# Kernel optimization log

Measured on AMD Instinct MI355X. Metric: run time of the kernel, lower is better.

The kernel has to match this reference:

```python
import jax, jax.numpy as jnp
import numpy as np

EPS = 1e-08


def _center(K):
    # H K H with H = I - 11^T/n, expressed as O(n^2) double mean-subtraction
    rm = K.mean(axis=-1, keepdims=True)
    cm = K.mean(axis=-2, keepdims=True)
    tm = K.mean(axis=(-1, -2), keepdims=True)
    return K - rm - cm + tm


def setup_inputs() -> dict:
    key = jax.random.key(0)
    k1, k2 = jax.random.split(key)
    L, B, n, d = 5, 8, 1024, 64
    teacher = jax.random.normal(k1, (L, B, n, d), dtype=jnp.float32)
    student = jax.random.normal(k2, (L, B, n, d), dtype=jnp.float32)
    return {"teacher": teacher, "student": student}


def reference(teacher, student):
    # teacher, student: [L, B, n, d]  (internal=True, dim>=3 branch)
    cX = _center(jnp.einsum('lbnd,lbmd->lbnm', teacher, teacher))  # [L,B,n,n]
    cY = _center(jnp.einsum('lbnd,lbmd->lbnm', student, student))  # [L,B,n,n]
    hsic_xy = jnp.sum(cX * cY, axis=(-1, -2))  # [L,B]
    var_x = jnp.sqrt(jnp.sum(cX * cX, axis=(-1, -2)))  # [L,B]
    var_y = jnp.sqrt(jnp.sum(cY * cY, axis=(-1, -2)))  # [L,B]
    ratio = jnp.abs(hsic_xy / (var_x * var_y))  # [L,B]
    loss_per_layer = -jnp.log(ratio.mean(axis=-1) + EPS)  # [L]
    return loss_per_layer.mean()  # sum over layers / length
```

## Files before the change

### kernel.cpp

```cpp
#include <hip/hip_runtime.h>
#include <math.h>

#define LL 5
#define BB 8
#define NN 1024
#define DD 64
#define LB (LL * BB)
#define SPLIT 8
#define ROWS (NN / SPLIT)
#define ZC (2 * DD)

#define G_SZ (LB * SPLIT * ZC * ZC)
#define S_SZ (LB * SPLIT * ZC)
#define ACC_OFF (G_SZ + S_SZ)

typedef short short8 __attribute__((ext_vector_type(8)));
typedef float floatx4 __attribute__((ext_vector_type(4)));

__device__ __forceinline__ unsigned short f2bf(float f) {
    union { float f; unsigned u; } v; v.f = f;
    const unsigned u = v.u;
    return (unsigned short)((u + 0x7FFFu + ((u >> 16) & 1u)) >> 16);
}

__device__ __forceinline__ short8 read_frag(const short* Zt, int t, int lane, int k0) {
    const int c = t + (lane & 15);
    const int o = (k0 >> 3) + (lane >> 4);
    return *(const short8*)(Zt + c * 128 + ((o ^ (c & 15)) << 3));
}

__global__ __launch_bounds__(256) void gram_kernel(const float* __restrict__ X,
                                                   const float* __restrict__ Y,
                                                   float* __restrict__ Gp,
                                                   float* __restrict__ Sp) {
    __shared__ short Zt[128 * 128];
    __shared__ float csum_sh[2][ZC];

    const int lb = blockIdx.y, nc = blockIdx.x, tid = threadIdx.x;
    const int c = tid & 127;
    const int half = tid >> 7;
    const int rbase = nc * ROWS;

    const float* src = (c < DD) ? (X + (size_t)lb * NN * DD + c)
                                : (Y + (size_t)lb * NN * DD + (c - DD));

#pragma unroll 4
    for (int j = 0; j < 32; ++j) {
        const int kp = half * 32 + j;
        const float v0 = src[(size_t)(rbase + 2 * kp) * DD];
        const float v1 = src[(size_t)(rbase + 2 * kp + 1) * DD];
        const unsigned val = (unsigned)f2bf(v0) | ((unsigned)f2bf(v1) << 16);
        const int o = kp >> 2, dw = kp & 3;
        *(unsigned*)((char*)Zt + (c << 8) + ((o ^ (c & 15)) << 4) + (dw << 2)) = val;
    }
    __syncthreads();

    {
        float s = 0.0f;
#pragma unroll
        for (int oo = 0; oo < 8; ++oo) {
            const int o = half * 8 + oo;
            const short8 v = *(const short8*)(Zt + c * 128 + ((o ^ (c & 15)) << 3));
#pragma unroll
            for (int e = 0; e < 8; ++e) {
                union { unsigned u; float f; } t2;
                t2.u = ((unsigned)(unsigned short)v[e]) << 16;
                s += t2.f;
            }
        }
        csum_sh[half][c] = s;
    }
    __syncthreads();
    if (tid < ZC) Sp[(lb * SPLIT + nc) * ZC + tid] = csum_sh[0][tid] + csum_sh[1][tid];

    const int lane = tid & 63, w = tid >> 6;
    const int wr = (w >> 1) * 64, wc = (w & 1) * 64;

    floatx4 acc[4][4];
#pragma unroll
    for (int i = 0; i < 4; ++i)
#pragma unroll
        for (int j = 0; j < 4; ++j)
            acc[i][j] = (floatx4){0.f, 0.f, 0.f, 0.f};

#pragma unroll
    for (int k0 = 0; k0 < ROWS; k0 += 32) {
        short8 af[4], bf_[4];
#pragma unroll
        for (int i = 0; i < 4; ++i) af[i] = read_frag(Zt, wr + i * 16, lane, k0);
#pragma unroll
        for (int j = 0; j < 4; ++j) bf_[j] = read_frag(Zt, wc + j * 16, lane, k0);
#pragma unroll
        for (int i = 0; i < 4; ++i)
#pragma unroll
            for (int j = 0; j < 4; ++j)
                acc[i][j] = __builtin_amdgcn_mfma_f32_16x16x32_bf16(af[i], bf_[j], acc[i][j], 0, 0, 0);
    }

    float* Gb = Gp + (size_t)(lb * SPLIT + nc) * (ZC * ZC);
    const int g = lane >> 4, cl = lane & 15;
#pragma unroll
    for (int i = 0; i < 4; ++i)
#pragma unroll
        for (int j = 0; j < 4; ++j)
#pragma unroll
            for (int r = 0; r < 4; ++r)
                Gb[(wr + i * 16 + g * 4 + r) * ZC + (wc + j * 16 + cl)] = acc[i][j][r];
}

__global__ __launch_bounds__(256) void reduce_kernel(const float* __restrict__ Gp,
                                                     const float* __restrict__ Sp,
                                                     float* __restrict__ Acc) {
    const int lb = blockIdx.x >> 2;
    const int q = blockIdx.x & 3;
    const int tid = threadIdx.x;
    __shared__ float s_sh[ZC];
    __shared__ float red[3][4];

    if (tid < ZC) {
        float s = 0.0f;
#pragma unroll
        for (int sp = 0; sp < SPLIT; ++sp) s += Sp[(lb * SPLIT + sp) * ZC + tid];
        s_sh[tid] = s;
    }
    __syncthreads();

    const float4* Gp4 = (const float4*)Gp;
    const size_t lb_base = (size_t)lb * SPLIT * (ZC * ZC / 4);
    float vxx = 0.0f, vyy = 0.0f, hxy = 0.0f;
    const float inv_n = 1.0f / (float)NN;
#pragma unroll
    for (int k = 0; k < 4; ++k) {
        const int e4 = q * 1024 + k * 256 + tid;
        float4 gsum = make_float4(0.f, 0.f, 0.f, 0.f);
#pragma unroll
        for (int sp = 0; sp < SPLIT; ++sp) {
            const float4 p = Gp4[lb_base + (size_t)sp * (ZC * ZC / 4) + e4];
            gsum.x += p.x; gsum.y += p.y; gsum.z += p.z; gsum.w += p.w;
        }
        const int i = e4 >> 5;
        const int j0 = (e4 & 31) << 2;
        const float si = s_sh[i] * inv_n;
        const float c0 = gsum.x - si * s_sh[j0 + 0];
        const float c1 = gsum.y - si * s_sh[j0 + 1];
        const float c2 = gsum.z - si * s_sh[j0 + 2];
        const float c3 = gsum.w - si * s_sh[j0 + 3];
        const float sq = c0 * c0 + c1 * c1 + c2 * c2 + c3 * c3;
        if (i < DD) {
            if (j0 < DD) vxx += sq;
            else         hxy += sq;
        } else {
            if (j0 >= DD) vyy += sq;
        }
    }
#pragma unroll
    for (int off = 32; off; off >>= 1) {
        vxx += __shfl_down(vxx, off);
        vyy += __shfl_down(vyy, off);
        hxy += __shfl_down(hxy, off);
    }
    const int wave = tid >> 6;
    if ((tid & 63) == 0) { red[0][wave] = vxx; red[1][wave] = vyy; red[2][wave] = hxy; }
    __syncthreads();
    if (tid == 0) {
        float a = 0.0f, b = 0.0f, h = 0.0f;
#pragma unroll
        for (int wv = 0; wv < 4; ++wv) { a += red[0][wv]; b += red[1][wv]; h += red[2][wv]; }
        atomicAdd(&Acc[lb * 4 + 0], a);
        atomicAdd(&Acc[lb * 4 + 1], b);
        atomicAdd(&Acc[lb * 4 + 2], h);
    }
}

__global__ void final_kernel(const float* __restrict__ Acc, float* __restrict__ out) {
    const int tid = threadIdx.x;
    float v = 0.0f;
    if (tid < LB) {
        const float a = Acc[tid * 4 + 0];
        const float b = Acc[tid * 4 + 1];
        const float h = Acc[tid * 4 + 2];
        v = fabsf(h / (sqrtf(a) * sqrtf(b)));
    }
    v += __shfl_xor(v, 1);
    v += __shfl_xor(v, 2);
    v += __shfl_xor(v, 4);
    float loss = 0.0f;
#pragma unroll
    for (int l = 0; l < LL; ++l) {
        const float sl = __shfl(v, l * BB);
        loss += -logf(sl * (1.0f / (float)BB) + 1e-8f);
    }
    if (tid == 0) out[0] = loss * (1.0f / (float)LL);
}

extern "C" void kernel_launch(void* const* d_in, const int* in_sizes, int n_in,
                              void* d_out, int out_size, void* d_ws, size_t ws_size,
                              hipStream_t stream) {
    const float* teacher = (const float*)d_in[0];
    const float* student = (const float*)d_in[1];
    float* ws = (float*)d_ws;
    float* Gp = ws;
    float* Sp = ws + G_SZ;
    float* Acc = ws + ACC_OFF;

    hipMemsetAsync(Acc, 0, LB * 4 * sizeof(float), stream);

    dim3 grid1(SPLIT, LB);
    gram_kernel<<<grid1, 256, 0, stream>>>(teacher, student, Gp, Sp);
    reduce_kernel<<<LB * 4, 256, 0, stream>>>(Gp, Sp, Acc);
    final_kernel<<<1, 64, 0, stream>>>(Acc, (float*)d_out);
}
```

Before: 79.75 us.

## Fuse split-K Gram and reduction into one block per batch with double buffering

```diff
diff --git a/kernel.cpp b/kernel.cpp
--- a/kernel.cpp
+++ b/kernel.cpp
@@ -6,13 +6,9 @@
 #define NN 1024
 #define DD 64
 #define LB (LL * BB)
-#define SPLIT 8
-#define ROWS (NN / SPLIT)
 #define ZC (2 * DD)
-
-#define G_SZ (LB * SPLIT * ZC * ZC)
-#define S_SZ (LB * SPLIT * ZC)
-#define ACC_OFF (G_SZ + S_SZ)
+#define CHUNK 128
+#define NCH (NN / CHUNK)
 
 typedef short short8 __attribute__((ext_vector_type(8)));
 typedef float floatx4 __attribute__((ext_vector_type(4)));
@@ -22,6 +18,9 @@
     const unsigned u = v.u;
     return (unsigned short)((u + 0x7FFFu + ((u >> 16) & 1u)) >> 16);
 }
+__device__ __forceinline__ float bf2f(unsigned short h) {
+    union { unsigned u; float f; } v; v.u = ((unsigned)h) << 16; return v.f;
+}
 
 __device__ __forceinline__ short8 read_frag(const short* Zt, int t, int lane, int k0) {
     const int c = t + (lane & 15);
@@ -29,52 +28,26 @@
     return *(const short8*)(Zt + c * 128 + ((o ^ (c & 15)) << 3));
 }
 
-__global__ __launch_bounds__(256) void gram_kernel(const float* __restrict__ X,
-                                                   const float* __restrict__ Y,
-                                                   float* __restrict__ Gp,
-                                                   float* __restrict__ Sp) {
-    __shared__ short Zt[128 * 128];
-    __shared__ float csum_sh[2][ZC];
+__global__ __launch_bounds__(512) void gram_fused(const float* __restrict__ X,
+                                                  const float* __restrict__ Y,
+                                                  float* __restrict__ R) {
+    __shared__ short Zt[2][CHUNK * ZC];
+    __shared__ float csum_sh[4][ZC];
+    __shared__ float stot[ZC];
+    __shared__ float red[4];
 
-    const int lb = blockIdx.y, nc = blockIdx.x, tid = threadIdx.x;
+    const int lb = blockIdx.x;
+    const int tid = threadIdx.x;
     const int c = tid & 127;
-    const int half = tid >> 7;
-    const int rbase = nc * ROWS;
+    const int qq = tid >> 7;
 
     const float* src = (c < DD) ? (X + (size_t)lb * NN * DD + c)
                                 : (Y + (size_t)lb * NN * DD + (c - DD));
 
-#pragma unroll 4
-    for (int j = 0; j < 32; ++j) {
-        const int kp = half * 32 + j;
-        const float v0 = src[(size_t)(rbase + 2 * kp) * DD];
-        const float v1 = src[(size_t)(rbase + 2 * kp + 1) * DD];
-        const unsigned val = (unsigned)f2bf(v0) | ((unsigned)f2bf(v1) << 16);
-        const int o = kp >> 2, dw = kp & 3;
-        *(unsigned*)((char*)Zt + (c << 8) + ((o ^ (c & 15)) << 4) + (dw << 2)) = val;
-    }
-    __syncthreads();
-
-    {
-        float s = 0.0f;
-#pragma unroll
-        for (int oo = 0; oo < 8; ++oo) {
-            const int o = half * 8 + oo;
-            const short8 v = *(const short8*)(Zt + c * 128 + ((o ^ (c & 15)) << 3));
-#pragma unroll
-            for (int e = 0; e < 8; ++e) {
-                union { unsigned u; float f; } t2;
-                t2.u = ((unsigned)(unsigned short)v[e]) << 16;
-                s += t2.f;
-            }
-        }
-        csum_sh[half][c] = s;
-    }
-    __syncthreads();
-    if (tid < ZC) Sp[(lb * SPLIT + nc) * ZC + tid] = csum_sh[0][tid] + csum_sh[1][tid];
-
     const int lane = tid & 63, w = tid >> 6;
-    const int wr = (w >> 1) * 64, wc = (w & 1) * 64;
+    const int qd = w & 3, hf = w >> 2;
+    const int wr = (qd >> 1) << 6;
+    const int wc_ = (qd & 1) << 6;
 
     floatx4 acc[4][4];
 #pragma unroll
@@ -82,105 +55,107 @@
 #pragma unroll
         for (int j = 0; j < 4; ++j)
             acc[i][j] = (floatx4){0.f, 0.f, 0.f, 0.f};
+    float csum = 0.0f;
 
+    {
+        short* Bn = Zt[0];
 #pragma unroll
-    for (int k0 = 0; k0 < ROWS; k0 += 32) {
-        short8 af[4], bf_[4];
+        for (int j = 0; j < 16; ++j) {
+            const int kp = qq * 16 + j;
+            const float v0 = src[(size_t)(2 * kp) * DD];
+            const float v1 = src[(size_t)(2 * kp + 1) * DD];
+            const unsigned short b0 = f2bf(v0), b1 = f2bf(v1);
+            csum += bf2f(b0) + bf2f(b1);
+            const unsigned val = (unsigned)b0 | ((unsigned)b1 << 16);
+            const int o = kp >> 2, dw = kp & 3;
+            *(unsigned*)((char*)Bn + (c << 8) + (((o ^ (c & 15)) << 4) + (dw << 2))) = val;
+        }
+    }
+    __syncthreads();
+
+    for (int ch = 0; ch < NCH; ++ch) {
+        const short* B = Zt[ch & 1];
+        if (ch + 1 < NCH) {
+            const int rbase = (ch + 1) * CHUNK;
+            short* Bn = Zt[(ch + 1) & 1];
 #pragma unroll
-        for (int i = 0; i < 4; ++i) af[i] = read_frag(Zt, wr + i * 16, lane, k0);
+            for (int j = 0; j < 16; ++j) {
+                const int kp = qq * 16 + j;
+                const float v0 = src[(size_t)(rbase + 2 * kp) * DD];
+                const float v1 = src[(size_t)(rbase + 2 * kp + 1) * DD];
+                const unsigned short b0 = f2bf(v0), b1 = f2bf(v1);
+                csum += bf2f(b0) + bf2f(b1);
+                const unsigned val = (unsigned)b0 | ((unsigned)b1 << 16);
+                const int o = kp >> 2, dw = kp & 3;
+                *(unsigned*)((char*)Bn + (c << 8) + (((o ^ (c & 15)) << 4) + (dw << 2))) = val;
+            }
+        }
 #pragma unroll
-        for (int j = 0; j < 4; ++j) bf_[j] = read_frag(Zt, wc + j * 16, lane, k0);
+        for (int s = 0; s < 2; ++s) {
+            const int k0 = hf * 64 + s * 32;
+            short8 af[4], bfr[4];
+#pragma unroll
+            for (int i = 0; i < 4; ++i) af[i] = read_frag(B, wr + i * 16, lane, k0);
+#pragma unroll
+            for (int j = 0; j < 4; ++j) bfr[j] = read_frag(B, wc_ + j * 16, lane, k0);
+#pragma unroll
+            for (int i = 0; i < 4; ++i)
+#pragma unroll
+                for (int j = 0; j < 4; ++j)
+                    acc[i][j] = __builtin_amdgcn_mfma_f32_16x16x32_bf16(af[i], bfr[j], acc[i][j], 0, 0, 0);
+        }
+        __syncthreads();
+    }
+
+    csum_sh[qq][c] = csum;
+    float* scr = (float*)Zt;
+    __syncthreads();
+
+    const int g = lane >> 4, cl = lane & 15;
+    if (hf == 0) {
 #pragma unroll
         for (int i = 0; i < 4; ++i)
 #pragma unroll
             for (int j = 0; j < 4; ++j)
-                acc[i][j] = __builtin_amdgcn_mfma_f32_16x16x32_bf16(af[i], bf_[j], acc[i][j], 0, 0, 0);
+#pragma unroll
+                for (int r = 0; r < 4; ++r)
+                    scr[qd * 4096 + (i * 16 + g * 4 + r) * 64 + (j * 16 + cl)] = acc[i][j][r];
     }
+    if (tid < ZC)
+        stot[tid] = csum_sh[0][tid] + csum_sh[1][tid] + csum_sh[2][tid] + csum_sh[3][tid];
+    __syncthreads();
 
-    float* Gb = Gp + (size_t)(lb * SPLIT + nc) * (ZC * ZC);
-    const int g = lane >> 4, cl = lane & 15;
+    if (hf == 1 && qd != 2) {
+        const float inv_n = 1.0f / (float)NN;
+        float sq = 0.0f;
 #pragma unroll
-    for (int i = 0; i < 4; ++i)
+        for (int i = 0; i < 4; ++i)
 #pragma unroll
-        for (int j = 0; j < 4; ++j)
+            for (int j = 0; j < 4; ++j) {
+                const int col = wc_ + j * 16 + cl;
+                const float sc = stot[col] * inv_n;
 #pragma unroll
-            for (int r = 0; r < 4; ++r)
-                Gb[(wr + i * 16 + g * 4 + r) * ZC + (wc + j * 16 + cl)] = acc[i][j][r];
-}
-
-__global__ __launch_bounds__(256) void reduce_kernel(const float* __restrict__ Gp,
-                                                     const float* __restrict__ Sp,
-                                                     float* __restrict__ Acc) {
-    const int lb = blockIdx.x >> 2;
-    const int q = blockIdx.x & 3;
-    const int tid = threadIdx.x;
-    __shared__ float s_sh[ZC];
-    __shared__ float red[3][4];
-
-    if (tid < ZC) {
-        float s = 0.0f;
+                for (int r = 0; r < 4; ++r) {
+                    const int row = wr + i * 16 + g * 4 + r;
+                    const float v = acc[i][j][r] + scr[qd * 4096 + (i * 16 + g * 4 + r) * 64 + (j * 16 + cl)];
+                    const float cv = v - stot[row] * sc;
+                    sq += cv * cv;
+                }
+            }
 #pragma unroll
-        for (int sp = 0; sp < SPLIT; ++sp) s += Sp[(lb * SPLIT + sp) * ZC + tid];
-        s_sh[tid] = s;
+        for (int off = 32; off; off >>= 1) sq += __shfl_down(sq, off);
+        if (lane == 0) red[qd] = sq;
     }
     __syncthreads();
-
-    const float4* Gp4 = (const float4*)Gp;
-    const size_t lb_base = (size_t)lb * SPLIT * (ZC * ZC / 4);
-    float vxx = 0.0f, vyy = 0.0f, hxy = 0.0f;
-    const float inv_n = 1.0f / (float)NN;
-#pragma unroll
-    for (int k = 0; k < 4; ++k) {
-        const int e4 = q * 1024 + k * 256 + tid;
-        float4 gsum = make_float4(0.f, 0.f, 0.f, 0.f);
-#pragma unroll
-        for (int sp = 0; sp < SPLIT; ++sp) {
-            const float4 p = Gp4[lb_base + (size_t)sp * (ZC * ZC / 4) + e4];
-            gsum.x += p.x; gsum.y += p.y; gsum.z += p.z; gsum.w += p.w;
-        }
-        const int i = e4 >> 5;
-        const int j0 = (e4 & 31) << 2;
-        const float si = s_sh[i] * inv_n;
-        const float c0 = gsum.x - si * s_sh[j0 + 0];
-        const float c1 = gsum.y - si * s_sh[j0 + 1];
-        const float c2 = gsum.z - si * s_sh[j0 + 2];
-        const float c3 = gsum.w - si * s_sh[j0 + 3];
-        const float sq = c0 * c0 + c1 * c1 + c2 * c2 + c3 * c3;
-        if (i < DD) {
-            if (j0 < DD) vxx += sq;
-            else         hxy += sq;
-        } else {
-            if (j0 >= DD) vyy += sq;
-        }
-    }
-#pragma unroll
-    for (int off = 32; off; off >>= 1) {
-        vxx += __shfl_down(vxx, off);
-        vyy += __shfl_down(vyy, off);
-        hxy += __shfl_down(hxy, off);
-    }
-    const int wave = tid >> 6;
-    if ((tid & 63) == 0) { red[0][wave] = vxx; red[1][wave] = vyy; red[2][wave] = hxy; }
-    __syncthreads();
     if (tid == 0) {
-        float a = 0.0f, b = 0.0f, h = 0.0f;
-#pragma unroll
-        for (int wv = 0; wv < 4; ++wv) { a += red[0][wv]; b += red[1][wv]; h += red[2][wv]; }
-        atomicAdd(&Acc[lb * 4 + 0], a);
-        atomicAdd(&Acc[lb * 4 + 1], b);
-        atomicAdd(&Acc[lb * 4 + 2], h);
+        const float vxx = red[0], hxy = red[1], vyy = red[3];
+        R[lb] = fabsf(hxy / (sqrtf(vxx) * sqrtf(vyy)));
     }
 }
 
-__global__ void final_kernel(const float* __restrict__ Acc, float* __restrict__ out) {
+__global__ void final_kernel(const float* __restrict__ R, float* __restrict__ out) {
     const int tid = threadIdx.x;
-    float v = 0.0f;
-    if (tid < LB) {
-        const float a = Acc[tid * 4 + 0];
-        const float b = Acc[tid * 4 + 1];
-        const float h = Acc[tid * 4 + 2];
-        v = fabsf(h / (sqrtf(a) * sqrtf(b)));
-    }
+    float v = (tid < LB) ? R[tid] : 0.0f;
     v += __shfl_xor(v, 1);
     v += __shfl_xor(v, 2);
     v += __shfl_xor(v, 4);
@@ -198,15 +173,8 @@
                               hipStream_t stream) {
     const float* teacher = (const float*)d_in[0];
     const float* student = (const float*)d_in[1];
-    float* ws = (float*)d_ws;
-    float* Gp = ws;
-    float* Sp = ws + G_SZ;
-    float* Acc = ws + ACC_OFF;
+    float* R = (float*)d_ws;
 
-    hipMemsetAsync(Acc, 0, LB * 4 * sizeof(float), stream);
-
-    dim3 grid1(SPLIT, LB);
-    gram_kernel<<<grid1, 256, 0, stream>>>(teacher, student, Gp, Sp);
-    reduce_kernel<<<LB * 4, 256, 0, stream>>>(Gp, Sp, Acc);
-    final_kernel<<<1, 64, 0, stream>>>(Acc, (float*)d_out);
+    gram_fused<<<LB, 512, 0, stream>>>(teacher, student, R);
+    final_kernel<<<1, 64, 0, stream>>>(R, (float*)d_out);
 }
```

New measurement: 81.57 us. +2.3%, slower.

## Double split count, coalesce loads, and store only three unique Gram quadrants

Applied to the files above, without the earlier changes.

```diff
diff --git a/kernel.cpp b/kernel.cpp
--- a/kernel.cpp
+++ b/kernel.cpp
@@ -6,13 +6,14 @@
 #define NN 1024
 #define DD 64
 #define LB (LL * BB)
-#define SPLIT 8
-#define ROWS (NN / SPLIT)
+#define SPLIT 16
+#define KC (NN / SPLIT)
 #define ZC (2 * DD)
-
-#define G_SZ (LB * SPLIT * ZC * ZC)
-#define S_SZ (LB * SPLIT * ZC)
-#define ACC_OFF (G_SZ + S_SZ)
+#define NQ 3
+
+#define GP_SZ (LB * SPLIT * NQ * 4096)
+#define SP_SZ (LB * SPLIT * ZC)
+#define ACC_OFF (GP_SZ + SP_SZ)
 
 typedef short short8 __attribute__((ext_vector_type(8)));
 typedef float floatx4 __attribute__((ext_vector_type(4)));
@@ -22,56 +23,59 @@
     const unsigned u = v.u;
     return (unsigned short)((u + 0x7FFFu + ((u >> 16) & 1u)) >> 16);
 }
-
-__device__ __forceinline__ short8 read_frag(const short* Zt, int t, int lane, int k0) {
-    const int c = t + (lane & 15);
+__device__ __forceinline__ float bf2f(unsigned short h) {
+    union { unsigned u; float f; } v; v.u = ((unsigned)h) << 16; return v.f;
+}
+
+__device__ __forceinline__ short8 read_frag(const short* Zt, int tbase, int lane, int k0) {
+    const int c = tbase + (lane & 15);
     const int o = (k0 >> 3) + (lane >> 4);
-    return *(const short8*)(Zt + c * 128 + ((o ^ (c & 15)) << 3));
+    return *(const short8*)(Zt + c * 64 + ((o ^ (c & 7)) << 3));
 }
 
 __global__ __launch_bounds__(256) void gram_kernel(const float* __restrict__ X,
                                                    const float* __restrict__ Y,
                                                    float* __restrict__ Gp,
                                                    float* __restrict__ Sp) {
-    __shared__ short Zt[128 * 128];
-    __shared__ float csum_sh[2][ZC];
+    __shared__ short Zt[ZC * KC];
+    __shared__ float cscr[8][ZC];
 
     const int lb = blockIdx.y, nc = blockIdx.x, tid = threadIdx.x;
-    const int c = tid & 127;
-    const int half = tid >> 7;
-    const int rbase = nc * ROWS;
-
-    const float* src = (c < DD) ? (X + (size_t)lb * NN * DD + c)
-                                : (Y + (size_t)lb * NN * DD + (c - DD));
-
-#pragma unroll 4
-    for (int j = 0; j < 32; ++j) {
-        const int kp = half * 32 + j;
-        const float v0 = src[(size_t)(rbase + 2 * kp) * DD];
-        const float v1 = src[(size_t)(rbase + 2 * kp + 1) * DD];
-        const unsigned val = (unsigned)f2bf(v0) | ((unsigned)f2bf(v1) << 16);
-        const int o = kp >> 2, dw = kp & 3;
-        *(unsigned*)((char*)Zt + (c << 8) + ((o ^ (c & 15)) << 4) + (dw << 2)) = val;
-    }
+    const int r0 = nc * KC;
+    const float4* X4 = (const float4*)(X + (size_t)lb * NN * DD);
+    const float4* Y4 = (const float4*)(Y + (size_t)lb * NN * DD);
+
+    const int col4 = tid & 31;
+    float4 v[8];
+#pragma unroll
+    for (int m = 0; m < 8; ++m) {
+        const int row = (tid >> 5) + 8 * m;
+        v[m] = (col4 < 16) ? X4[(size_t)(r0 + row) * 16 + col4]
+                           : Y4[(size_t)(r0 + row) * 16 + (col4 - 16)];
+    }
+
+    float cs[4] = {0.f, 0.f, 0.f, 0.f};
+#pragma unroll
+    for (int m = 0; m < 8; ++m) {
+        const int k = (tid >> 5) + 8 * m;
+        const float a[4] = {v[m].x, v[m].y, v[m].z, v[m].w};
+#pragma unroll
+        for (int e = 0; e < 4; ++e) {
+            const int c = 4 * col4 + e;
+            const unsigned short b = f2bf(a[e]);
+            cs[e] += bf2f(b);
+            Zt[c * 64 + (((k >> 3) ^ (c & 7)) << 3) + (k & 7)] = (short)b;
+        }
+    }
+#pragma unroll
+    for (int e = 0; e < 4; ++e) cscr[tid >> 5][4 * col4 + e] = cs[e];
     __syncthreads();
-
-    {
-        float s = 0.0f;
-#pragma unroll
-        for (int oo = 0; oo < 8; ++oo) {
-            const int o = half * 8 + oo;
-            const short8 v = *(const short8*)(Zt + c * 128 + ((o ^ (c & 15)) << 3));
-#pragma unroll
-            for (int e = 0; e < 8; ++e) {
-                union { unsigned u; float f; } t2;
-                t2.u = ((unsigned)(unsigned short)v[e]) << 16;
-                s += t2.f;
-            }
-        }
-        csum_sh[half][c] = s;
-    }
-    __syncthreads();
-    if (tid < ZC) Sp[(lb * SPLIT + nc) * ZC + tid] = csum_sh[0][tid] + csum_sh[1][tid];
+    if (tid < ZC) {
+        float s = 0.f;
+#pragma unroll
+        for (int g = 0; g < 8; ++g) s += cscr[g][tid];
+        Sp[(lb * SPLIT + nc) * ZC + tid] = s;
+    }
 
     const int lane = tid & 63, w = tid >> 6;
     const int wr = (w >> 1) * 64, wc = (w & 1) * 64;
@@ -80,96 +84,83 @@
 #pragma unroll
     for (int i = 0; i < 4; ++i)
 #pragma unroll
-        for (int j = 0; j < 4; ++j)
-            acc[i][j] = (floatx4){0.f, 0.f, 0.f, 0.f};
-
-#pragma unroll
-    for (int k0 = 0; k0 < ROWS; k0 += 32) {
-        short8 af[4], bf_[4];
+        for (int j = 0; j < 4; ++j) acc[i][j] = (floatx4){0.f, 0.f, 0.f, 0.f};
+
+#pragma unroll
+    for (int k0 = 0; k0 < KC; k0 += 32) {
+        short8 af[4], bfr[4];
 #pragma unroll
         for (int i = 0; i < 4; ++i) af[i] = read_frag(Zt, wr + i * 16, lane, k0);
 #pragma unroll
-        for (int j = 0; j < 4; ++j) bf_[j] = read_frag(Zt, wc + j * 16, lane, k0);
+        for (int j = 0; j < 4; ++j) bfr[j] = read_frag(Zt, wc + j * 16, lane, k0);
 #pragma unroll
         for (int i = 0; i < 4; ++i)
 #pragma unroll
             for (int j = 0; j < 4; ++j)
-                acc[i][j] = __builtin_amdgcn_mfma_f32_16x16x32_bf16(af[i], bf_[j], acc[i][j], 0, 0, 0);
-    }
-
-    float* Gb = Gp + (size_t)(lb * SPLIT + nc) * (ZC * ZC);
-    const int g = lane >> 4, cl = lane & 15;
-#pragma unroll
-    for (int i = 0; i < 4; ++i)
-#pragma unroll
-        for (int j = 0; j < 4; ++j)
-#pragma unroll
-            for (int r = 0; r < 4; ++r)
-                Gb[(wr + i * 16 + g * 4 + r) * ZC + (wc + j * 16 + cl)] = acc[i][j][r];
+                acc[i][j] = __builtin_amdgcn_mfma_f32_16x16x32_bf16(af[i], bfr[j], acc[i][j], 0, 0, 0);
+    }
+
+    if (w != 2) {
+        const int slot = (w == 0) ? 0 : (w == 1) ? 1 : 2;
+        float* Gb = Gp + ((size_t)(lb * SPLIT + nc) * NQ + slot) * 4096;
+        const int g = lane >> 4, cl = lane & 15;
+#pragma unroll
+        for (int i = 0; i < 4; ++i)
+#pragma unroll
+            for (int j = 0; j < 4; ++j)
+#pragma unroll
+                for (int r = 0; r < 4; ++r)
+                    Gb[(i * 16 + g * 4 + r) * 64 + (j * 16 + cl)] = acc[i][j][r];
+    }
 }
 
 __global__ __launch_bounds__(256) void reduce_kernel(const float* __restrict__ Gp,
                                                      const float* __restrict__ Sp,
                                                      float* __restrict__ Acc) {
-    const int lb = blockIdx.x >> 2;
-    const int q = blockIdx.x & 3;
+    const int b = blockIdx.x;
+    const int lb = b / (NQ * 4);
+    const int rem = b % (NQ * 4);
+    const int q = rem >> 2, seg = rem & 3;
     const int tid = threadIdx.x;
-    __shared__ float s_sh[ZC];
-    __shared__ float red[3][4];
+
+    __shared__ float stot[ZC];
+    __shared__ float red[4];
 
     if (tid < ZC) {
-        float s = 0.0f;
+        float s = 0.f;
 #pragma unroll
         for (int sp = 0; sp < SPLIT; ++sp) s += Sp[(lb * SPLIT + sp) * ZC + tid];
-        s_sh[tid] = s;
+        stot[tid] = s;
     }
     __syncthreads();
 
-    const float4* Gp4 = (const float4*)Gp;
-    const size_t lb_base = (size_t)lb * SPLIT * (ZC * ZC / 4);
-    float vxx = 0.0f, vyy = 0.0f, hxy = 0.0f;
+    const int rowbase = (q == 2) ? 64 : 0;
+    const int colbase = (q == 0) ? 0 : 64;
+    const int idx0 = seg * 1024 + tid * 4;
+
+    float4 g = make_float4(0.f, 0.f, 0.f, 0.f);
+#pragma unroll
+    for (int sp = 0; sp < SPLIT; ++sp) {
+        const float4 p = *(const float4*)&Gp[((size_t)(lb * SPLIT + sp) * NQ + q) * 4096 + idx0];
+        g.x += p.x; g.y += p.y; g.z += p.z; g.w += p.w;
+    }
+    const int row = idx0 >> 6, colb = idx0 & 63;
     const float inv_n = 1.0f / (float)NN;
-#pragma unroll
-    for (int k = 0; k < 4; ++k) {
-        const int e4 = q * 1024 + k * 256 + tid;
-        float4 gsum = make_float4(0.f, 0.f, 0.f, 0.f);
-#pragma unroll
-        for (int sp = 0; sp < SPLIT; ++sp) {
-            const float4 p = Gp4[lb_base + (size_t)sp * (ZC * ZC / 4) + e4];
-            gsum.x += p.x; gsum.y += p.y; gsum.z += p.z; gsum.w += p.w;
-        }
-        const int i = e4 >> 5;
-        const int j0 = (e4 & 31) << 2;
-        const float si = s_sh[i] * inv_n;
-        const float c0 = gsum.x - si * s_sh[j0 + 0];
-        const float c1 = gsum.y - si * s_sh[j0 + 1];
-        const float c2 = gsum.z - si * s_sh[j0 + 2];
-        const float c3 = gsum.w - si * s_sh[j0 + 3];
-        const float sq = c0 * c0 + c1 * c1 + c2 * c2 + c3 * c3;
-        if (i < DD) {
-            if (j0 < DD) vxx += sq;
-            else         hxy += sq;
-        } else {
-            if (j0 >= DD) vyy += sq;
-        }
-    }
-#pragma unroll
-    for (int off = 32; off; off >>= 1) {
-        vxx += __shfl_down(vxx, off);
-        vyy += __shfl_down(vyy, off);
-        hxy += __shfl_down(hxy, off);
-    }
+    const float srow = stot[rowbase + row] * inv_n;
+    const float ga[4] = {g.x, g.y, g.z, g.w};
+    float sq = 0.f;
+#pragma unroll
+    for (int e = 0; e < 4; ++e) {
+        const float cv = ga[e] - srow * stot[colbase + colb + e];
+        sq += cv * cv;
+    }
+#pragma unroll
+    for (int off = 32; off; off >>= 1) sq += __shfl_down(sq, off);
     const int wave = tid >> 6;
-    if ((tid & 63) == 0) { red[0][wave] = vxx; red[1][wave] = vyy; red[2][wave] = hxy; }
+    if ((tid & 63) == 0) red[wave] = sq;
     __syncthreads();
-    if (tid == 0) {
-        float a = 0.0f, b = 0.0f, h = 0.0f;
-#pragma unroll
-        for (int wv = 0; wv < 4; ++wv) { a += red[0][wv]; b += red[1][wv]; h += red[2][wv]; }
-        atomicAdd(&Acc[lb * 4 + 0], a);
-        atomicAdd(&Acc[lb * 4 + 1], b);
-        atomicAdd(&Acc[lb * 4 + 2], h);
-    }
+    if (tid == 0)
+        atomicAdd(&Acc[lb * 4 + q], red[0] + red[1] + red[2] + red[3]);
 }
 
 __global__ void final_kernel(const float* __restrict__ Acc, float* __restrict__ out) {
@@ -177,9 +168,9 @@
     float v = 0.0f;
     if (tid < LB) {
         const float a = Acc[tid * 4 + 0];
-        const float b = Acc[tid * 4 + 1];
-        const float h = Acc[tid * 4 + 2];
-        v = fabsf(h / (sqrtf(a) * sqrtf(b)));
+        const float h = Acc[tid * 4 + 1];
+        const float bb = Acc[tid * 4 + 2];
+        v = fabsf(h / (sqrtf(a) * sqrtf(bb)));
     }
     v += __shfl_xor(v, 1);
     v += __shfl_xor(v, 2);
@@ -200,13 +191,13 @@
     const float* student = (const float*)d_in[1];
     float* ws = (float*)d_ws;
     float* Gp = ws;
-    float* Sp = ws + G_SZ;
+    float* Sp = ws + GP_SZ;
     float* Acc = ws + ACC_OFF;
 
     hipMemsetAsync(Acc, 0, LB * 4 * sizeof(float), stream);
 
     dim3 grid1(SPLIT, LB);
     gram_kernel<<<grid1, 256, 0, stream>>>(teacher, student, Gp, Sp);
-    reduce_kernel<<<LB * 4, 256, 0, stream>>>(Gp, Sp, Acc);
+    reduce_kernel<<<LB * NQ * 4, 256, 0, stream>>>(Gp, Sp, Acc);
     final_kernel<<<1, 64, 0, stream>>>(Acc, (float*)d_out);
 }
```

Result: slower. 82.62 us (+3.6%).
